# Kernel optimization log

Measured on AMD Instinct MI355X. Metric: run time of the kernel, lower is better.

Reference implementation:

```python
import jax, jax.numpy as jnp
import numpy as np

B, L, D, H = 4, 8192, 1024, 8
Dh = D // H
EPS = 1e-4
PAD = 1  # circular padding on each side, kernel_size=3, stride=1


def setup_inputs() -> dict:
    key = jax.random.key(0)
    k1, k2, k3, k4, k5 = jax.random.split(key, 5)
    return {
        "x": jax.random.normal(k1, (B, L, D), dtype=jnp.float32),
        "hash_w": jax.random.normal(k2, (H, Dh, 2), dtype=jnp.float32) * 0.05,
        "hash_b": jax.random.normal(k3, (H, 2), dtype=jnp.float32) * 0.05,
        "conv_w": jax.random.normal(k4, (D, D // H, 3), dtype=jnp.float32) * 0.05,
        "conv_b": jax.random.normal(k5, (D,), dtype=jnp.float32) * 0.05,
    }


def reference(x, hash_w, hash_b, conv_w, conv_b):
    # x: [B, L, D]
    xh = x.reshape(B, L, H, Dh)
    # per-head 2-dim hash projection, concatenated as [x0,y0,x1,y1,...] on last dim
    proj = jnp.einsum('blhd,hdk->blhk', xh, hash_w) + hash_b  # [B,L,H,2]
    proj = proj.reshape(B, L, 2 * H)
    # faithful to torch.split(projected, n_heads, dim=2): first H vs last H channels
    h_x, h_y = proj[..., :H], proj[..., H:]
    angles = jnp.arctan(h_x / (h_y + EPS))  # [B,L,H]
    idx = jnp.argsort(angles, axis=1)       # [B,L,H] permutation along L per (b,h)
    # gather: reorder tokens per head
    xs = jnp.take_along_axis(xh, idx[..., None], axis=1)  # [B,L,H,Dh]
    # grouped circular Conv1d over the sorted sequence
    xc = xs.reshape(B, L, D).swapaxes(1, 2)               # [B,D,L]
    xc = jnp.pad(xc, ((0, 0), (0, 0), (PAD, PAD)), mode='wrap')
    y = jax.lax.conv_general_dilated(
        xc, conv_w, window_strides=(1,), padding='VALID',
        dimension_numbers=('NCH', 'OIH', 'NCH'), feature_group_count=H)
    y = y + conv_b[None, :, None]                          # [B,D,L]
    y = y.swapaxes(1, 2).reshape(B, L, H, Dh)
    # scatter back to original token order == gather with inverse permutation
    inv = jnp.argsort(idx, axis=1)
    out = jnp.take_along_axis(y, inv[..., None], axis=1)
    return out.reshape(B, L, D)
```

## Files before the change

### kernel.cpp

```cpp
#include <hip/hip_runtime.h>
#include <math.h>

#define LL 8192
#define DD 1024
#define DH 128

typedef unsigned long long u64;
typedef __attribute__((ext_vector_type(8))) short bf16x8;
typedef __attribute__((ext_vector_type(4))) float f32x4;

__device__ __forceinline__ unsigned short f2bf(float f) {
  unsigned u = __float_as_uint(f);
  u = (u + 0x7fffu + ((u >> 16) & 1u)) >> 16;
  return (unsigned short)u;
}

__device__ __forceinline__ float fdlibm_atanf(float x) {
#pragma clang fp contract(off)
  const float atanhi0 = __uint_as_float(0x3eed6338u);
  const float atanhi1 = __uint_as_float(0x3f490fdau);
  const float atanhi2 = __uint_as_float(0x3f7b985eu);
  const float atanhi3 = __uint_as_float(0x3fc90fdau);
  const float atanlo0 = __uint_as_float(0x31ac3769u);
  const float atanlo1 = __uint_as_float(0x33222168u);
  const float atanlo2 = __uint_as_float(0x33140fb4u);
  const float atanlo3 = __uint_as_float(0x33a22168u);
  const float aT0 = __uint_as_float(0x3eaaaaa9u);
  const float aT1 = __uint_as_float(0xbe4cca98u);
  const float aT2 = __uint_as_float(0x3e11f50du);
  const float aT3 = __uint_as_float(0xbdda1247u);
  const float aT4 = __uint_as_float(0x3d7cac25u);
  unsigned hx = __float_as_uint(x);
  unsigned ix = hx & 0x7fffffffu;
  int id;
  if (ix >= 0x4c800000u) {
    if (ix > 0x7f800000u) return x + x;
    float z = atanhi3 + atanlo3;
    return (hx >> 31) ? -z : z;
  }
  if (ix < 0x3ee00000u) {
    if (ix < 0x39800000u) return x;
    id = -1;
  } else {
    x = fabsf(x);
    if (ix < 0x3f980000u) {
      if (ix < 0x3f300000u) { id = 0; x = (2.0f * x - 1.0f) / (2.0f + x); }
      else                  { id = 1; x = (x - 1.0f) / (x + 1.0f); }
    } else {
      if (ix < 0x401c0000u) { id = 2; x = (x - 1.5f) / (1.0f + 1.5f * x); }
      else                  { id = 3; x = -1.0f / x; }
    }
  }
  float z = x * x;
  float w = z * z;
  float s1 = z * (aT0 + w * (aT2 + w * aT4));
  float s2 = w * (aT1 + w * aT3);
  if (id < 0) return x - x * (s1 + s2);
  float r;
  if (id == 0)      r = atanhi0 - ((x * (s1 + s2) - atanlo0) - x);
  else if (id == 1) r = atanhi1 - ((x * (s1 + s2) - atanlo1) - x);
  else if (id == 2) r = atanhi2 - ((x * (s1 + s2) - atanlo2) - x);
  else              r = atanhi3 - ((x * (s1 + s2) - atanlo3) - x);
  return (hx >> 31) ? -r : r;
}

__global__ __launch_bounds__(256) void k_keys(const float* __restrict__ x,
                                              const float* __restrict__ hw,
                                              const float* __restrict__ hb,
                                              u64* __restrict__ ks) {
  __shared__ float2 wL[128][8];
  __shared__ float projL[32][16];
  const int tid = threadIdx.x;
  const float2* hw2 = (const float2*)hw;
  for (int i = tid; i < 1024; i += 256) {
    int hh = i >> 7, dd = i & 127;
    wL[dd][hh] = hw2[i];
  }
  __syncthreads();
  const int r = tid >> 3;
  const int h = tid & 7;
  const int m = blockIdx.x * 32 + r;
  const float4* xp = (const float4*)(x + (size_t)m * DD + h * DH);
  float a0 = 0.f, a1 = 0.f;
#pragma unroll
  for (int q = 0; q < 32; ++q) {
    float4 v = xp[q];
    float2 w0 = wL[q * 4 + 0][h];
    float2 w1 = wL[q * 4 + 1][h];
    float2 w2 = wL[q * 4 + 2][h];
    float2 w3 = wL[q * 4 + 3][h];
    a0 = fmaf(v.x, w0.x, a0); a1 = fmaf(v.x, w0.y, a1);
    a0 = fmaf(v.y, w1.x, a0); a1 = fmaf(v.y, w1.y, a1);
    a0 = fmaf(v.z, w2.x, a0); a1 = fmaf(v.z, w2.y, a1);
    a0 = fmaf(v.w, w3.x, a0); a1 = fmaf(v.w, w3.y, a1);
  }
  projL[r][h * 2 + 0] = a0;
  projL[r][h * 2 + 1] = a1;
  __syncthreads();
  const int j = h;
  float px = projL[r][j] + hb[j];
  float py = projL[r][8 + j] + hb[8 + j];
  float den = py + 1e-4f;
  float ratio = px / den;
  float angle = fdlibm_atanf(ratio);
  unsigned am = __float_as_uint(angle);
  am = (am & 0x80000000u) ? ~am : (am | 0x80000000u);
  const int b = m >> 13, l = m & (LL - 1);
  ks[((size_t)b * 8 + j) * LL + l] = ((u64)am << 13) | (u64)l;
}

__global__ __launch_bounds__(1024) void k_sort_loc(u64* __restrict__ ks) {
  __shared__ u64 sk[2048];
  const int blk = blockIdx.x;
  const int seg = blk >> 2, c = blk & 3;
  u64* base = ks + (size_t)seg * LL + c * 2048;
  const int tid = threadIdx.x;
  sk[tid] = base[tid];
  sk[tid + 1024] = base[tid + 1024];
  __syncthreads();
  const int cb = c * 2048;
  for (int size = 2; size <= 2048; size <<= 1) {
    for (int stride = size >> 1; stride > 0; stride >>= 1) {
      int i = 2 * tid - (tid & (stride - 1));
      int j = i + stride;
      bool up = (((cb + i) & size) == 0);
      u64 a = sk[i], d = sk[j];
      if ((a > d) == up) { sk[i] = d; sk[j] = a; }
      __syncthreads();
    }
  }
  base[tid] = sk[tid];
  base[tid + 1024] = sk[tid + 1024];
}

__global__ __launch_bounds__(256) void k_sort_glob(u64* __restrict__ ks,
                                                   int size, int stride) {
  int t = blockIdx.x * 256 + threadIdx.x;
  int seg = t >> 12, p = t & 4095;
  int i = 2 * p - (p & (stride - 1));
  int j = i + stride;
  u64* base = ks + (size_t)seg * LL;
  bool up = ((i & size) == 0);
  u64 a = base[i], d = base[j];
  if ((a > d) == up) { base[i] = d; base[j] = a; }
}

__global__ __launch_bounds__(1024) void k_sort_tail(u64* __restrict__ ks,
                                                    int size,
                                                    int* __restrict__ perm) {
  __shared__ u64 sk[2048];
  const int blk = blockIdx.x;
  const int seg = blk >> 2, c = blk & 3;
  u64* base = ks + (size_t)seg * LL + c * 2048;
  const int tid = threadIdx.x;
  sk[tid] = base[tid];
  sk[tid + 1024] = base[tid + 1024];
  __syncthreads();
  const int cb = c * 2048;
  for (int stride = 1024; stride > 0; stride >>= 1) {
    int i = 2 * tid - (tid & (stride - 1));
    int j = i + stride;
    bool up = (((cb + i) & size) == 0);
    u64 a = sk[i], d = sk[j];
    if ((a > d) == up) { sk[i] = d; sk[j] = a; }
    __syncthreads();
  }
  if (perm) {
    int* dst = perm + (size_t)seg * LL + c * 2048;
    dst[tid] = (int)(sk[tid] & (u64)(LL - 1));
    dst[tid + 1024] = (int)(sk[tid + 1024] & (u64)(LL - 1));
  } else {
    base[tid] = sk[tid];
    base[tid + 1024] = sk[tid + 1024];
  }
}

__global__ __launch_bounds__(256) void k_wt(const float* __restrict__ cw,
                                            unsigned short* __restrict__ wb) {
  int g = blockIdx.x * 256 + threadIdx.x;
  if (g >= 8 * 12 * 8 * 64 * 8) return;
  int h = g / 49152;
  int rem = g % 49152;
  int kk = rem >> 12;
  int rem2 = rem & 4095;
  int n = rem2 >> 9;
  int rem3 = rem2 & 511;
  int l = rem3 >> 3;
  int j = rem3 & 7;
  int k = kk * 32 + ((l >> 4) * 8) + j;
  int o = n * 16 + (l & 15);
  int t = k >> 7, i = k & 127;
  wb[g] = f2bf(cw[((size_t)(h * 128 + o)) * 384 + i * 3 + t]);
}

__global__ __launch_bounds__(256) void k_conv(const float* __restrict__ x,
                                              const unsigned short* __restrict__ wb,
                                              const float* __restrict__ bias,
                                              const int* __restrict__ perm,
                                              float* __restrict__ out) {
  __shared__ short Xs[66 * 136];
  __shared__ short Ws[8 * 64 * 8];
  __shared__ int Ps[64];
  const int tid = threadIdx.x;
  const int bid = blockIdx.x;
  const int tile = bid & 127;
  const int h = (bid >> 7) & 7;
  const int b = bid >> 10;
  const int r0 = tile * 64;
  const int* pbh = perm + ((size_t)b * 8 + h) * LL;
  if (tid < 64) Ps[tid] = pbh[r0 + tid];
  {
    const int ln = tid & 31;
    for (int j = (tid >> 5); j < 66; j += 8) {
      int rank = (r0 + j - 1 + LL) & (LL - 1);
      int src = pbh[rank];
      float4 v = ((const float4*)(x + ((size_t)(b * LL + src)) * DD + h * DH))[ln];
      uint2 pk;
      pk.x = (unsigned)f2bf(v.x) | ((unsigned)f2bf(v.y) << 16);
      pk.y = (unsigned)f2bf(v.z) | ((unsigned)f2bf(v.w) << 16);
      *(uint2*)(Xs + j * 136 + ln * 4) = pk;
    }
  }
  const int w = tid >> 6;
  const int l = tid & 63;
  const int arow = w * 16 + (l & 15);
  const int acol = (l >> 4) * 8;
  f32x4 acc[8];
#pragma unroll
  for (int n = 0; n < 8; ++n) acc[n] = (f32x4){0.f, 0.f, 0.f, 0.f};
  const uint4* wsrc = (const uint4*)(wb + (size_t)h * 49152);
  uint4* Ws16 = (uint4*)Ws;
  for (int kk = 0; kk < 12; ++kk) {
    __syncthreads();
    Ws16[tid] = wsrc[kk * 512 + tid];
    Ws16[tid + 256] = wsrc[kk * 512 + tid + 256];
    __syncthreads();
    bf16x8 af = *(const bf16x8*)(Xs + (arow + (kk >> 2)) * 136 + (kk & 3) * 32 + acol);
#pragma unroll
    for (int n = 0; n < 8; ++n) {
      bf16x8 bf_ = *(const bf16x8*)(Ws + (n * 64 + l) * 8);
      acc[n] = __builtin_amdgcn_mfma_f32_16x16x32_bf16(af, bf_, acc[n], 0, 0, 0);
    }
  }
  int dsts[4];
#pragma unroll
  for (int reg = 0; reg < 4; ++reg) dsts[reg] = Ps[w * 16 + (l >> 4) * 4 + reg];
#pragma unroll
  for (int n = 0; n < 8; ++n) {
    int o = h * DH + n * 16 + (l & 15);
    float bv = bias[o];
#pragma unroll
    for (int reg = 0; reg < 4; ++reg) {
      out[((size_t)(b * LL + dsts[reg])) * DD + o] = acc[n][reg] + bv;
    }
  }
}

extern "C" void kernel_launch(void* const* d_in, const int* in_sizes, int n_in,
                              void* d_out, int out_size, void* d_ws, size_t ws_size,
                              hipStream_t stream) {
  const float* x  = (const float*)d_in[0];
  const float* hw = (const float*)d_in[1];
  const float* hb = (const float*)d_in[2];
  const float* cw = (const float*)d_in[3];
  const float* cb = (const float*)d_in[4];
  float* out = (float*)d_out;
  u64* ks   = (u64*)d_ws;
  int* perm = (int*)((char*)d_ws + (2u << 20));
  unsigned short* wbp = (unsigned short*)((char*)d_ws + (3u << 20));

  k_keys<<<1024, 256, 0, stream>>>(x, hw, hb, ks);
  k_wt<<<1536, 256, 0, stream>>>(cw, wbp);
  k_sort_loc<<<128, 1024, 0, stream>>>(ks);
  k_sort_glob<<<512, 256, 0, stream>>>(ks, 4096, 2048);
  k_sort_tail<<<128, 1024, 0, stream>>>(ks, 4096, nullptr);
  k_sort_glob<<<512, 256, 0, stream>>>(ks, 8192, 4096);
  k_sort_glob<<<512, 256, 0, stream>>>(ks, 8192, 2048);
  k_sort_tail<<<128, 1024, 0, stream>>>(ks, 8192, perm);
  k_conv<<<4096, 256, 0, stream>>>(x, wbp, cb, perm, out);
}
```

Baseline: 125.6 us.

## Merge bitonic sort passes and enlarge conv tiles with double-buffered weights

```diff
diff --git a/kernel.cpp b/kernel.cpp
--- a/kernel.cpp
+++ b/kernel.cpp
@@ -133,16 +133,43 @@
   base[tid + 1024] = sk[tid + 1024];
 }
 
-__global__ __launch_bounds__(256) void k_sort_glob(u64* __restrict__ ks,
-                                                   int size, int stride) {
+__global__ __launch_bounds__(1024) void k_sort_t4k(u64* __restrict__ ks) {
+  __shared__ u64 sk[4096];
+  const int blk = blockIdx.x;
+  const int seg = blk >> 1, c = blk & 1;
+  u64* base = ks + (size_t)seg * LL + c * 4096;
+  const int tid = threadIdx.x;
+#pragma unroll
+  for (int i = 0; i < 4; ++i) sk[tid + i * 1024] = base[tid + i * 1024];
+  __syncthreads();
+  const int cb = c * 4096;
+  for (int stride = 2048; stride > 0; stride >>= 1) {
+#pragma unroll
+    for (int pp = 0; pp < 2; ++pp) {
+      int p = tid + pp * 1024;
+      int i = 2 * p - (p & (stride - 1));
+      int j = i + stride;
+      bool up = (((cb + i) & 4096) == 0);
+      u64 a = sk[i], d = sk[j];
+      if ((a > d) == up) { sk[i] = d; sk[j] = a; }
+    }
+    __syncthreads();
+  }
+#pragma unroll
+  for (int i = 0; i < 4; ++i) base[tid + i * 1024] = sk[tid + i * 1024];
+}
+
+__global__ __launch_bounds__(256) void k_sort_g8(u64* __restrict__ ks) {
   int t = blockIdx.x * 256 + threadIdx.x;
-  int seg = t >> 12, p = t & 4095;
-  int i = 2 * p - (p & (stride - 1));
-  int j = i + stride;
+  int seg = t >> 11, i = t & 2047;
   u64* base = ks + (size_t)seg * LL;
-  bool up = ((i & size) == 0);
-  u64 a = base[i], d = base[j];
-  if ((a > d) == up) { base[i] = d; base[j] = a; }
+  u64 e0 = base[i], e1 = base[i + 2048], e2 = base[i + 4096], e3 = base[i + 6144];
+  u64 tt;
+  if (e0 > e2) { tt = e0; e0 = e2; e2 = tt; }
+  if (e1 > e3) { tt = e1; e1 = e3; e3 = tt; }
+  if (e0 > e1) { tt = e0; e0 = e1; e1 = tt; }
+  if (e2 > e3) { tt = e2; e2 = e3; e3 = tt; }
+  base[i] = e0; base[i + 2048] = e1; base[i + 4096] = e2; base[i + 6144] = e3;
 }
 
 __global__ __launch_bounds__(1024) void k_sort_tail(u64* __restrict__ ks,
@@ -198,20 +225,26 @@
                                               const float* __restrict__ bias,
                                               const int* __restrict__ perm,
                                               float* __restrict__ out) {
-  __shared__ short Xs[66 * 136];
-  __shared__ short Ws[8 * 64 * 8];
-  __shared__ int Ps[64];
+  __shared__ short Xs[130 * 136];
+  __shared__ short Ws[2][8 * 64 * 8];
+  __shared__ int Ps[128];
   const int tid = threadIdx.x;
   const int bid = blockIdx.x;
-  const int tile = bid & 127;
-  const int h = (bid >> 7) & 7;
-  const int b = bid >> 10;
-  const int r0 = tile * 64;
+  const int tile = bid & 63;
+  const int h = (bid >> 6) & 7;
+  const int b = bid >> 9;
+  const int r0 = tile * 128;
   const int* pbh = perm + ((size_t)b * 8 + h) * LL;
-  if (tid < 64) Ps[tid] = pbh[r0 + tid];
+  if (tid < 128) Ps[tid] = pbh[r0 + tid];
+  const uint4* wsrc = (const uint4*)(wb + (size_t)h * 49152);
+  {
+    uint4* W0 = (uint4*)Ws[0];
+    W0[tid] = wsrc[tid];
+    W0[tid + 256] = wsrc[tid + 256];
+  }
   {
     const int ln = tid & 31;
-    for (int j = (tid >> 5); j < 66; j += 8) {
+    for (int j = (tid >> 5); j < 130; j += 8) {
       int rank = (r0 + j - 1 + LL) & (LL - 1);
       int src = pbh[rank];
       float4 v = ((const float4*)(x + ((size_t)(b * LL + src)) * DD + h * DH))[ln];
@@ -223,35 +256,46 @@
   }
   const int w = tid >> 6;
   const int l = tid & 63;
-  const int arow = w * 16 + (l & 15);
+  const int arow = w * 32 + (l & 15);
   const int acol = (l >> 4) * 8;
-  f32x4 acc[8];
-#pragma unroll
-  for (int n = 0; n < 8; ++n) acc[n] = (f32x4){0.f, 0.f, 0.f, 0.f};
-  const uint4* wsrc = (const uint4*)(wb + (size_t)h * 49152);
-  uint4* Ws16 = (uint4*)Ws;
+  f32x4 acc[2][8];
+#pragma unroll
+  for (int tt = 0; tt < 2; ++tt)
+#pragma unroll
+    for (int n = 0; n < 8; ++n) acc[tt][n] = (f32x4){0.f, 0.f, 0.f, 0.f};
+  __syncthreads();
   for (int kk = 0; kk < 12; ++kk) {
+    const int cur = kk & 1;
+    if (kk < 11) {
+      uint4* Wn = (uint4*)Ws[cur ^ 1];
+      Wn[tid] = wsrc[(kk + 1) * 512 + tid];
+      Wn[tid + 256] = wsrc[(kk + 1) * 512 + tid + 256];
+    }
+    const short* xrow = Xs + (arow + (kk >> 2)) * 136 + (kk & 3) * 32 + acol;
+    bf16x8 af0 = *(const bf16x8*)(xrow);
+    bf16x8 af1 = *(const bf16x8*)(xrow + 16 * 136);
+#pragma unroll
+    for (int n = 0; n < 8; ++n) {
+      bf16x8 bfr = *(const bf16x8*)(Ws[cur] + (n * 64 + l) * 8);
+      acc[0][n] = __builtin_amdgcn_mfma_f32_16x16x32_bf16(af0, bfr, acc[0][n], 0, 0, 0);
+      acc[1][n] = __builtin_amdgcn_mfma_f32_16x16x32_bf16(af1, bfr, acc[1][n], 0, 0, 0);
+    }
     __syncthreads();
-    Ws16[tid] = wsrc[kk * 512 + tid];
-    Ws16[tid + 256] = wsrc[kk * 512 + tid + 256];
-    __syncthreads();
-    bf16x8 af = *(const bf16x8*)(Xs + (arow + (kk >> 2)) * 136 + (kk & 3) * 32 + acol);
+  }
+#pragma unroll
+  for (int tt = 0; tt < 2; ++tt) {
+    int dsts[4];
+#pragma unroll
+    for (int reg = 0; reg < 4; ++reg)
+      dsts[reg] = Ps[w * 32 + tt * 16 + (l >> 4) * 4 + reg];
 #pragma unroll
     for (int n = 0; n < 8; ++n) {
-      bf16x8 bf_ = *(const bf16x8*)(Ws + (n * 64 + l) * 8);
-      acc[n] = __builtin_amdgcn_mfma_f32_16x16x32_bf16(af, bf_, acc[n], 0, 0, 0);
-    }
-  }
-  int dsts[4];
-#pragma unroll
-  for (int reg = 0; reg < 4; ++reg) dsts[reg] = Ps[w * 16 + (l >> 4) * 4 + reg];
-#pragma unroll
-  for (int n = 0; n < 8; ++n) {
-    int o = h * DH + n * 16 + (l & 15);
-    float bv = bias[o];
-#pragma unroll
-    for (int reg = 0; reg < 4; ++reg) {
-      out[((size_t)(b * LL + dsts[reg])) * DD + o] = acc[n][reg] + bv;
+      int o = h * DH + n * 16 + (l & 15);
+      float bv = bias[o];
+#pragma unroll
+      for (int reg = 0; reg < 4; ++reg) {
+        out[((size_t)(b * LL + dsts[reg])) * DD + o] = acc[tt][n][reg] + bv;
+      }
     }
   }
 }
@@ -272,10 +316,8 @@
   k_keys<<<1024, 256, 0, stream>>>(x, hw, hb, ks);
   k_wt<<<1536, 256, 0, stream>>>(cw, wbp);
   k_sort_loc<<<128, 1024, 0, stream>>>(ks);
-  k_sort_glob<<<512, 256, 0, stream>>>(ks, 4096, 2048);
-  k_sort_tail<<<128, 1024, 0, stream>>>(ks, 4096, nullptr);
-  k_sort_glob<<<512, 256, 0, stream>>>(ks, 8192, 4096);
-  k_sort_glob<<<512, 256, 0, stream>>>(ks, 8192, 2048);
+  k_sort_t4k<<<64, 1024, 0, stream>>>(ks);
+  k_sort_g8<<<256, 256, 0, stream>>>(ks);
   k_sort_tail<<<128, 1024, 0, stream>>>(ks, 8192, perm);
-  k_conv<<<4096, 256, 0, stream>>>(x, wbp, cb, perm, out);
-}
+  k_conv<<<2048, 256, 0, stream>>>(x, wbp, cb, perm, out);
+}
```

Measured after the change: 151.8 us. 20.9% more time.

## Restructure bitonic sort stages and fold weight conversion into key kernel

Applied to the files above, without the earlier changes.

```diff
diff --git a/kernel.cpp b/kernel.cpp
--- a/kernel.cpp
+++ b/kernel.cpp
@@ -67,7 +67,9 @@
 __global__ __launch_bounds__(256) void k_keys(const float* __restrict__ x,
                                               const float* __restrict__ hw,
                                               const float* __restrict__ hb,
-                                              u64* __restrict__ ks) {
+                                              u64* __restrict__ ks,
+                                              const float* __restrict__ cw,
+                                              unsigned short* __restrict__ wb) {
   __shared__ float2 wL[128][8];
   __shared__ float projL[32][16];
   const int tid = threadIdx.x;
@@ -107,19 +109,36 @@
   am = (am & 0x80000000u) ? ~am : (am | 0x80000000u);
   const int b = m >> 13, l = m & (LL - 1);
   ks[((size_t)b * 8 + j) * LL + l] = ((u64)am << 13) | (u64)l;
-}
-
-__global__ __launch_bounds__(1024) void k_sort_loc(u64* __restrict__ ks) {
-  __shared__ u64 sk[2048];
+  {
+    int base = blockIdx.x * 384;
+    for (int g = base + tid; g < base + 384; g += 256) {
+      int hh = g / 49152;
+      int rem = g % 49152;
+      int kk = rem >> 12;
+      int rem2 = rem & 4095;
+      int n = rem2 >> 9;
+      int rem3 = rem2 & 511;
+      int l2 = rem3 >> 3;
+      int j2 = rem3 & 7;
+      int k = kk * 32 + ((l2 >> 4) * 8) + j2;
+      int o = n * 16 + (l2 & 15);
+      int t = k >> 7, i2 = k & 127;
+      wb[g] = f2bf(cw[((size_t)(hh * 128 + o)) * 384 + i2 * 3 + t]);
+    }
+  }
+}
+
+__global__ __launch_bounds__(256) void k_sort_loc512(u64* __restrict__ ks) {
+  __shared__ u64 sk[512];
   const int blk = blockIdx.x;
-  const int seg = blk >> 2, c = blk & 3;
-  u64* base = ks + (size_t)seg * LL + c * 2048;
+  const int seg = blk >> 4, c = blk & 15;
+  u64* base = ks + (size_t)seg * LL + c * 512;
   const int tid = threadIdx.x;
   sk[tid] = base[tid];
-  sk[tid + 1024] = base[tid + 1024];
-  __syncthreads();
-  const int cb = c * 2048;
-  for (int size = 2; size <= 2048; size <<= 1) {
+  sk[tid + 256] = base[tid + 256];
+  __syncthreads();
+  const int cb = c * 512;
+  for (int size = 2; size <= 512; size <<= 1) {
     for (int stride = size >> 1; stride > 0; stride >>= 1) {
       int i = 2 * tid - (tid & (stride - 1));
       int j = i + stride;
@@ -130,19 +149,70 @@
     }
   }
   base[tid] = sk[tid];
+  base[tid + 256] = sk[tid + 256];
+}
+
+__global__ __launch_bounds__(1024) void k_sort_loc2k(u64* __restrict__ ks) {
+  __shared__ u64 sk[2048];
+  const int blk = blockIdx.x;
+  const int seg = blk >> 2, c = blk & 3;
+  u64* base = ks + (size_t)seg * LL + c * 2048;
+  const int tid = threadIdx.x;
+  sk[tid] = base[tid];
+  sk[tid + 1024] = base[tid + 1024];
+  __syncthreads();
+  const int cb = c * 2048;
+  for (int size = 1024; size <= 2048; size <<= 1) {
+    for (int stride = size >> 1; stride > 0; stride >>= 1) {
+      int i = 2 * tid - (tid & (stride - 1));
+      int j = i + stride;
+      bool up = (((cb + i) & size) == 0);
+      u64 a = sk[i], d = sk[j];
+      if ((a > d) == up) { sk[i] = d; sk[j] = a; }
+      __syncthreads();
+    }
+  }
+  base[tid] = sk[tid];
   base[tid + 1024] = sk[tid + 1024];
 }
 
-__global__ __launch_bounds__(256) void k_sort_glob(u64* __restrict__ ks,
-                                                   int size, int stride) {
+__global__ __launch_bounds__(1024) void k_sort_t4k(u64* __restrict__ ks) {
+  __shared__ u64 sk[4096];
+  const int blk = blockIdx.x;
+  const int seg = blk >> 1, c = blk & 1;
+  u64* base = ks + (size_t)seg * LL + c * 4096;
+  const int tid = threadIdx.x;
+#pragma unroll
+  for (int i = 0; i < 4; ++i) sk[tid + i * 1024] = base[tid + i * 1024];
+  __syncthreads();
+  const int cb = c * 4096;
+  for (int stride = 2048; stride > 0; stride >>= 1) {
+#pragma unroll
+    for (int pp = 0; pp < 2; ++pp) {
+      int p = tid + pp * 1024;
+      int i = 2 * p - (p & (stride - 1));
+      int j = i + stride;
+      bool up = (((cb + i) & 4096) == 0);
+      u64 a = sk[i], d = sk[j];
+      if ((a > d) == up) { sk[i] = d; sk[j] = a; }
+    }
+    __syncthreads();
+  }
+#pragma unroll
+  for (int i = 0; i < 4; ++i) base[tid + i * 1024] = sk[tid + i * 1024];
+}
+
+__global__ __launch_bounds__(256) void k_sort_g8(u64* __restrict__ ks) {
   int t = blockIdx.x * 256 + threadIdx.x;
-  int seg = t >> 12, p = t & 4095;
-  int i = 2 * p - (p & (stride - 1));
-  int j = i + stride;
+  int seg = t >> 11, i = t & 2047;
   u64* base = ks + (size_t)seg * LL;
-  bool up = ((i & size) == 0);
-  u64 a = base[i], d = base[j];
-  if ((a > d) == up) { base[i] = d; base[j] = a; }
+  u64 e0 = base[i], e1 = base[i + 2048], e2 = base[i + 4096], e3 = base[i + 6144];
+  u64 tt;
+  if (e0 > e2) { tt = e0; e0 = e2; e2 = tt; }
+  if (e1 > e3) { tt = e1; e1 = e3; e3 = tt; }
+  if (e0 > e1) { tt = e0; e0 = e1; e1 = tt; }
+  if (e2 > e3) { tt = e2; e2 = e3; e3 = tt; }
+  base[i] = e0; base[i + 2048] = e1; base[i + 4096] = e2; base[i + 6144] = e3;
 }
 
 __global__ __launch_bounds__(1024) void k_sort_tail(u64* __restrict__ ks,
@@ -173,24 +243,6 @@
     base[tid] = sk[tid];
     base[tid + 1024] = sk[tid + 1024];
   }
-}
-
-__global__ __launch_bounds__(256) void k_wt(const float* __restrict__ cw,
-                                            unsigned short* __restrict__ wb) {
-  int g = blockIdx.x * 256 + threadIdx.x;
-  if (g >= 8 * 12 * 8 * 64 * 8) return;
-  int h = g / 49152;
-  int rem = g % 49152;
-  int kk = rem >> 12;
-  int rem2 = rem & 4095;
-  int n = rem2 >> 9;
-  int rem3 = rem2 & 511;
-  int l = rem3 >> 3;
-  int j = rem3 & 7;
-  int k = kk * 32 + ((l >> 4) * 8) + j;
-  int o = n * 16 + (l & 15);
-  int t = k >> 7, i = k & 127;
-  wb[g] = f2bf(cw[((size_t)(h * 128 + o)) * 384 + i * 3 + t]);
 }
 
 __global__ __launch_bounds__(256) void k_conv(const float* __restrict__ x,
@@ -269,13 +321,11 @@
   int* perm = (int*)((char*)d_ws + (2u << 20));
   unsigned short* wbp = (unsigned short*)((char*)d_ws + (3u << 20));
 
-  k_keys<<<1024, 256, 0, stream>>>(x, hw, hb, ks);
-  k_wt<<<1536, 256, 0, stream>>>(cw, wbp);
-  k_sort_loc<<<128, 1024, 0, stream>>>(ks);
-  k_sort_glob<<<512, 256, 0, stream>>>(ks, 4096, 2048);
-  k_sort_tail<<<128, 1024, 0, stream>>>(ks, 4096, nullptr);
-  k_sort_glob<<<512, 256, 0, stream>>>(ks, 8192, 4096);
-  k_sort_glob<<<512, 256, 0, stream>>>(ks, 8192, 2048);
+  k_keys<<<1024, 256, 0, stream>>>(x, hw, hb, ks, cw, wbp);
+  k_sort_loc512<<<512, 256, 0, stream>>>(ks);
+  k_sort_loc2k<<<128, 1024, 0, stream>>>(ks);
+  k_sort_t4k<<<64, 1024, 0, stream>>>(ks);
+  k_sort_g8<<<256, 256, 0, stream>>>(ks);
   k_sort_tail<<<128, 1024, 0, stream>>>(ks, 8192, perm);
   k_conv<<<4096, 256, 0, stream>>>(x, wbp, cb, perm, out);
 }
```

Measured after the change: 122.4 us. -2.5%, faster.
